# Optimization experiments

Measured on AMD Instinct MI355X. Metric: run time of the kernel, lower is better.

The kernel has to match this reference:

```python
import jax, jax.numpy as jnp
import numpy as np

B, T, H, F = 32, 2048, 1024, 1024  # batch, kv_len, hidden_size, feature_size


def setup_inputs() -> dict:
    key = jax.random.key(0)
    ks = jax.random.split(key, 6)
    s = 0.02  # param init scale
    return {
        "query": jax.random.normal(ks[0], (B, 1, H), jnp.float32),
        "keys": jax.random.normal(ks[1], (B, T, F), jnp.float32),
        "Wa_w": jax.random.normal(ks[2], (H, H), jnp.float32) * s,
        "Wa_b": jnp.zeros((H,), jnp.float32),
        "Ua_w": jax.random.normal(ks[3], (H, F), jnp.float32) * s,
        "Ua_b": jnp.zeros((H,), jnp.float32),
        "Va_w": jax.random.normal(ks[4], (1, H), jnp.float32) * s,
        "Va_b": jnp.zeros((1,), jnp.float32),
    }


def reference(query, keys, Wa_w, Wa_b, Ua_w, Ua_b, Va_w, Va_b):
    # Wa(query): [B,1,H]; Ua(keys): [B,T,H]
    q = jnp.einsum('bqh,oh->bqo', query, Wa_w) + Wa_b
    k = jnp.einsum('btf,of->bto', keys, Ua_w) + Ua_b
    e = jnp.tanh(q + k)                                   # [B,T,H] (broadcast over q dim of size 1)
    scores = jnp.einsum('bth,h->bt', e, Va_w[0]) + Va_b[0]  # Va(...).squeeze(2) -> [B,T]
    scores = scores[:, None, :]                           # unsqueeze(1) -> [B,1,T]
    weights = jax.nn.softmax(scores, axis=-1)             # [B,1,T]
    context = jnp.einsum('bqt,btf->bqf', weights, keys)   # bmm -> [B,1,F]
    return context, weights
```

## Files before the change

### kernel.cpp

```cpp
#include <hip/hip_runtime.h>
#include <hip/hip_bf16.h>

typedef float  f32x4 __attribute__((ext_vector_type(4)));
typedef short  s16x8 __attribute__((ext_vector_type(8)));
typedef __hip_bfloat16 bf16;

#define BDIM 32
#define TDIM 2048
#define HDIM 1024
#define FDIM 1024
#define MTOT (BDIM*TDIM)

#define GLOAD16(gp, lp) __builtin_amdgcn_global_load_lds(                     \
    (const __attribute__((address_space(1))) void*)(gp),                      \
    (__attribute__((address_space(3))) void*)(lp), 16, 0, 0)

#define MFMA_BF16 __builtin_amdgcn_mfma_f32_16x16x32_bf16

__global__ __launch_bounds__(256) void cvt_bf16_kernel(
    const float* __restrict__ src, bf16* __restrict__ dst, int n8)
{
    int i = blockIdx.x * 256 + threadIdx.x;
    const int stride = gridDim.x * 256;
    for (; i < n8; i += stride) {
        const f32x4 a = ((const f32x4*)src)[2 * i];
        const f32x4 b = ((const f32x4*)src)[2 * i + 1];
        union { bf16 h[8]; s16x8 v; } u;
        #pragma unroll
        for (int j = 0; j < 4; ++j) {
            u.h[j]     = __float2bfloat16(a[j]);
            u.h[4 + j] = __float2bfloat16(b[j]);
        }
        ((s16x8*)dst)[i] = u.v;
    }
}

__global__ __launch_bounds__(256) void qeff_kernel(
    const float* __restrict__ query, const float* __restrict__ Wa_w,
    const float* __restrict__ Wa_b,  const float* __restrict__ Ua_b,
    float* __restrict__ qe)
{
    const int lane = threadIdx.x & 63;
    const int gw   = blockIdx.x * 4 + (threadIdx.x >> 6);
    const int b    = gw >> 10;
    const int o    = gw & 1023;
    const float* qp = query + (size_t)b * HDIM;
    const float* wp = Wa_w  + (size_t)o * HDIM;
    float s = 0.f;
    #pragma unroll
    for (int i = 0; i < 16; ++i) {
        const int h = i * 64 + lane;
        s += qp[h] * wp[h];
    }
    #pragma unroll
    for (int off = 32; off > 0; off >>= 1) s += __shfl_down(s, off);
    if (lane == 0) qe[gw] = s + Wa_b[o] + Ua_b[o];
}

#define STAGE_A(buf_, kb_, h_, s_) GLOAD16(                                    \
    Ab + (size_t)(M0 + (h_)*128 + (((s_)>>1)<<4) + srow) * FDIM               \
       + (kb_) + (((s_)&1)<<5) + scg*8,                                        \
    &As[buf_][((((h_)*8 + ((s_)>>1)) * 2 + ((s_)&1)) << 9)])
#define STAGE_B(buf_, kb_, h_, s_) GLOAD16(                                    \
    Bb + (size_t)(N0 + (h_)*128 + (((s_)>>1)<<4) + srow) * FDIM               \
       + (kb_) + (((s_)&1)<<5) + scg*8,                                        \
    &Bs[buf_][((((h_)*8 + ((s_)>>1)) * 2 + ((s_)&1)) << 9)])

__global__ __launch_bounds__(512) void score_gemm_256_kernel(
    const bf16* __restrict__ Ab, const bf16* __restrict__ Bb,
    const float* __restrict__ qe, const float* __restrict__ Va,
    float* __restrict__ scores)
{
    __shared__ bf16 As[2][16384];
    __shared__ bf16 Bs[2][16384];

    const int tid  = threadIdx.x;
    const int lane = tid & 63;
    const int w    = tid >> 6;
    const int wr   = w >> 2;
    const int wc   = w & 3;

    const int bid   = blockIdx.x;
    const int local = bid >> 3;
    const int mt    = (bid & 7) * 32 + (local >> 2);
    const int nt    = local & 3;
    const int M0 = mt * 256, N0 = nt * 256;

    const int srow = lane >> 2;
    const int scg  = (lane & 3) ^ (((lane >> 5) & 1) << 1);
    const int r    = lane & 15;
    const int q4   = lane >> 4;
    const int roff = r * 32 + ((q4 ^ (((r >> 3) & 1) << 1)) & 3) * 8;

    f32x4 acc[8][4];
    #pragma unroll
    for (int m = 0; m < 8; ++m)
        #pragma unroll
        for (int n = 0; n < 4; ++n) acc[m][n] = (f32x4){0.f, 0.f, 0.f, 0.f};

    STAGE_B(0, 0, 0, w); STAGE_B(0, 0, 0, w + 8);
    STAGE_B(0, 0, 1, w); STAGE_B(0, 0, 1, w + 8);
    STAGE_A(0, 0, 0, w); STAGE_A(0, 0, 0, w + 8);
    STAGE_A(0, 0, 1, w); STAGE_A(0, 0, 1, w + 8);
    STAGE_B(1, 64, 0, w); STAGE_B(1, 64, 0, w + 8);
    STAGE_B(1, 64, 1, w); STAGE_B(1, 64, 1, w + 8);
    STAGE_A(1, 64, 0, w); STAGE_A(1, 64, 0, w + 8);
    STAGE_A(1, 64, 1, w); STAGE_A(1, 64, 1, w + 8);
    asm volatile("s_waitcnt vmcnt(8)" ::: "memory");
    __builtin_amdgcn_s_barrier();

    for (int i = 0; i < 8; ++i) {
        const bool pf  = (i < 7);
        const int kbe = (2 * i + 2) << 6;
        const int kbo = (2 * i + 3) << 6;

        s16x8 a0[4][2], a1[4][2], b0[2][2], b1[2][2];

        #pragma unroll
        for (int mf = 0; mf < 4; ++mf)
            #pragma unroll
            for (int ks = 0; ks < 2; ++ks)
                a0[mf][ks] = *(const s16x8*)
                    &As[0][(((wr * 8 + mf) * 2 + ks) << 9) + roff];
        #pragma unroll
        for (int nf = 0; nf < 2; ++nf)
            #pragma unroll
            for (int ks = 0; ks < 2; ++ks)
                b0[nf][ks] = *(const s16x8*)
                    &Bs[0][(((wc * 4 + nf) * 2 + ks) << 9) + roff];
        __builtin_amdgcn_s_barrier();
        __builtin_amdgcn_s_setprio(1);
        #pragma unroll
        for (int mf = 0; mf < 4; ++mf)
            #pragma unroll
            for (int nf = 0; nf < 2; ++nf)
                #pragma unroll
                for (int ks = 0; ks < 2; ++ks)
                    acc[mf][nf] = MFMA_BF16(a0[mf][ks], b0[nf][ks],
                                            acc[mf][nf], 0, 0, 0);
        __builtin_amdgcn_s_setprio(0);
        __builtin_amdgcn_s_barrier();

        #pragma unroll
        for (int nf = 0; nf < 2; ++nf)
            #pragma unroll
            for (int ks = 0; ks < 2; ++ks)
                b1[nf][ks] = *(const s16x8*)
                    &Bs[0][(((wc * 4 + 2 + nf) * 2 + ks) << 9) + roff];
        __builtin_amdgcn_s_barrier();
        __builtin_amdgcn_s_setprio(1);
        #pragma unroll
        for (int mf = 0; mf < 4; ++mf)
            #pragma unroll
            for (int nf = 0; nf < 2; ++nf)
                #pragma unroll
                for (int ks = 0; ks < 2; ++ks)
                    acc[mf][2 + nf] = MFMA_BF16(a0[mf][ks], b1[nf][ks],
                                                acc[mf][2 + nf], 0, 0, 0);
        __builtin_amdgcn_s_setprio(0);
        __builtin_amdgcn_s_barrier();

        #pragma unroll
        for (int mf = 0; mf < 4; ++mf)
            #pragma unroll
            for (int ks = 0; ks < 2; ++ks)
                a1[mf][ks] = *(const s16x8*)
                    &As[0][(((wr * 8 + 4 + mf) * 2 + ks) << 9) + roff];
        if (pf) {
            STAGE_B(0, kbe, 0, w); STAGE_B(0, kbe, 0, w + 8);
            STAGE_B(0, kbe, 1, w); STAGE_B(0, kbe, 1, w + 8);
        }
        __builtin_amdgcn_s_barrier();
        __builtin_amdgcn_s_setprio(1);
        #pragma unroll
        for (int mf = 0; mf < 4; ++mf)
            #pragma unroll
            for (int nf = 0; nf < 2; ++nf)
                #pragma unroll
                for (int ks = 0; ks < 2; ++ks)
                    acc[4 + mf][nf] = MFMA_BF16(a1[mf][ks], b0[nf][ks],
                                                acc[4 + mf][nf], 0, 0, 0);
        __builtin_amdgcn_s_setprio(0);
        __builtin_amdgcn_s_barrier();

        if (pf) {
            STAGE_A(0, kbe, 0, w); STAGE_A(0, kbe, 0, w + 8);
            STAGE_A(0, kbe, 1, w); STAGE_A(0, kbe, 1, w + 8);
        }
        __builtin_amdgcn_s_barrier();
        __builtin_amdgcn_s_setprio(1);
        #pragma unroll
        for (int mf = 0; mf < 4; ++mf)
            #pragma unroll
            for (int nf = 0; nf < 2; ++nf)
                #pragma unroll
                for (int ks = 0; ks < 2; ++ks)
                    acc[4 + mf][2 + nf] = MFMA_BF16(a1[mf][ks], b1[nf][ks],
                                                    acc[4 + mf][2 + nf], 0, 0, 0);
        __builtin_amdgcn_s_setprio(0);
        if (pf) asm volatile("s_waitcnt vmcnt(8)" ::: "memory");
        else    asm volatile("s_waitcnt vmcnt(0)" ::: "memory");
        __builtin_amdgcn_s_barrier();

        #pragma unroll
        for (int mf = 0; mf < 4; ++mf)
            #pragma unroll
            for (int ks = 0; ks < 2; ++ks)
                a0[mf][ks] = *(const s16x8*)
                    &As[1][(((wr * 8 + mf) * 2 + ks) << 9) + roff];
        #pragma unroll
        for (int nf = 0; nf < 2; ++nf)
            #pragma unroll
            for (int ks = 0; ks < 2; ++ks)
                b0[nf][ks] = *(const s16x8*)
                    &Bs[1][(((wc * 4 + nf) * 2 + ks) << 9) + roff];
        __builtin_amdgcn_s_barrier();
        __builtin_amdgcn_s_setprio(1);
        #pragma unroll
        for (int mf = 0; mf < 4; ++mf)
            #pragma unroll
            for (int nf = 0; nf < 2; ++nf)
                #pragma unroll
                for (int ks = 0; ks < 2; ++ks)
                    acc[mf][nf] = MFMA_BF16(a0[mf][ks], b0[nf][ks],
                                            acc[mf][nf], 0, 0, 0);
        __builtin_amdgcn_s_setprio(0);
        __builtin_amdgcn_s_barrier();

        #pragma unroll
        for (int nf = 0; nf < 2; ++nf)
            #pragma unroll
            for (int ks = 0; ks < 2; ++ks)
                b1[nf][ks] = *(const s16x8*)
                    &Bs[1][(((wc * 4 + 2 + nf) * 2 + ks) << 9) + roff];
        __builtin_amdgcn_s_barrier();
        __builtin_amdgcn_s_setprio(1);
        #pragma unroll
        for (int mf = 0; mf < 4; ++mf)
            #pragma unroll
            for (int nf = 0; nf < 2; ++nf)
                #pragma unroll
                for (int ks = 0; ks < 2; ++ks)
                    acc[mf][2 + nf] = MFMA_BF16(a0[mf][ks], b1[nf][ks],
                                                acc[mf][2 + nf], 0, 0, 0);
        __builtin_amdgcn_s_setprio(0);
        __builtin_amdgcn_s_barrier();

        #pragma unroll
        for (int mf = 0; mf < 4; ++mf)
            #pragma unroll
            for (int ks = 0; ks < 2; ++ks)
                a1[mf][ks] = *(const s16x8*)
                    &As[1][(((wr * 8 + 4 + mf) * 2 + ks) << 9) + roff];
        if (pf) {
            STAGE_B(1, kbo, 0, w); STAGE_B(1, kbo, 0, w + 8);
            STAGE_B(1, kbo, 1, w); STAGE_B(1, kbo, 1, w + 8);
        }
        __builtin_amdgcn_s_barrier();
        __builtin_amdgcn_s_setprio(1);
        #pragma unroll
        for (int mf = 0; mf < 4; ++mf)
            #pragma unroll
            for (int nf = 0; nf < 2; ++nf)
                #pragma unroll
                for (int ks = 0; ks < 2; ++ks)
                    acc[4 + mf][nf] = MFMA_BF16(a1[mf][ks], b0[nf][ks],
                                                acc[4 + mf][nf], 0, 0, 0);
        __builtin_amdgcn_s_setprio(0);
        __builtin_amdgcn_s_barrier();

        if (pf) {
            STAGE_A(1, kbo, 0, w); STAGE_A(1, kbo, 0, w + 8);
            STAGE_A(1, kbo, 1, w); STAGE_A(1, kbo, 1, w + 8);
        }
        __builtin_amdgcn_s_barrier();
        __builtin_amdgcn_s_setprio(1);
        #pragma unroll
        for (int mf = 0; mf < 4; ++mf)
            #pragma unroll
            for (int nf = 0; nf < 2; ++nf)
                #pragma unroll
                for (int ks = 0; ks < 2; ++ks)
                    acc[4 + mf][2 + nf] = MFMA_BF16(a1[mf][ks], b1[nf][ks],
                                                    acc[4 + mf][2 + nf], 0, 0, 0);
        __builtin_amdgcn_s_setprio(0);
        if (pf) asm volatile("s_waitcnt vmcnt(8)" ::: "memory");
        __builtin_amdgcn_s_barrier();
    }

    const int b = M0 >> 11;
    const float* qrow = qe + (size_t)b * HDIM;
    #pragma unroll
    for (int mf = 0; mf < 8; ++mf) {
        float part[4] = {0.f, 0.f, 0.f, 0.f};
        #pragma unroll
        for (int nf = 0; nf < 4; ++nf) {
            const int c    = N0 + wc * 64 + nf * 16 + (lane & 15);
            const float va = Va[c];
            const float qv = qrow[c];
            #pragma unroll
            for (int j = 0; j < 4; ++j) {
                const float x = qv + acc[mf][nf][j];
                const float e = __expf(2.0f * x);
                part[j] += va * (1.0f - 2.0f / (e + 1.0f));
            }
        }
        #pragma unroll
        for (int j = 0; j < 4; ++j)
            #pragma unroll
            for (int off = 1; off < 16; off <<= 1)
                part[j] += __shfl_xor(part[j], off);
        if ((lane & 15) == 0) {
            const int rr = M0 + wr * 128 + mf * 16 + (lane >> 4) * 4;
            #pragma unroll
            for (int j = 0; j < 4; ++j) atomicAdd(&scores[rr + j], part[j]);
        }
    }
}

__global__ __launch_bounds__(256) void score_gemm_f32_kernel(
    const float* __restrict__ keys, const float* __restrict__ Ua,
    const float* __restrict__ qe,   const float* __restrict__ Va,
    float* __restrict__ scores)
{
    __shared__ bf16 Asf[128][40];
    __shared__ bf16 Bsf[128][40];

    const int tid  = threadIdx.x;
    const int lane = tid & 63;
    const int wid  = tid >> 6;
    const int wr   = wid >> 1, wc = wid & 1;
    const int n0   = blockIdx.x * 128;
    const int m0   = blockIdx.y * 128;

    const int srow  = tid >> 1;
    const int shalf = tid & 1;
    const float* gA = keys + (size_t)(m0 + srow) * FDIM + shalf * 16;
    const float* gB = Ua   + (size_t)(n0 + srow) * FDIM + shalf * 16;

    f32x4 acc[4][4];
    #pragma unroll
    for (int m = 0; m < 4; ++m)
        #pragma unroll
        for (int n = 0; n < 4; ++n) acc[m][n] = (f32x4){0.f, 0.f, 0.f, 0.f};

    float4 ra[4], rbv[4];
    #pragma unroll
    for (int i = 0; i < 4; ++i) {
        ra[i]  = ((const float4*)gA)[i];
        rbv[i] = ((const float4*)gB)[i];
    }

    for (int kt = 0; kt < 32; ++kt) {
        __syncthreads();
        {
            union { bf16 h[16]; s16x8 v[2]; } ua, ub;
            #pragma unroll
            for (int i = 0; i < 4; ++i) {
                const float* fa = (const float*)&ra[i];
                const float* fb = (const float*)&rbv[i];
                #pragma unroll
                for (int j = 0; j < 4; ++j) {
                    ua.h[i*4+j] = __float2bfloat16(fa[j]);
                    ub.h[i*4+j] = __float2bfloat16(fb[j]);
                }
            }
            *(s16x8*)&Asf[srow][shalf*16]     = ua.v[0];
            *(s16x8*)&Asf[srow][shalf*16 + 8] = ua.v[1];
            *(s16x8*)&Bsf[srow][shalf*16]     = ub.v[0];
            *(s16x8*)&Bsf[srow][shalf*16 + 8] = ub.v[1];
        }
        __syncthreads();

        if (kt + 1 < 32) {
            const float* pa = gA + (kt + 1) * 32;
            const float* pb = gB + (kt + 1) * 32;
            #pragma unroll
            for (int i = 0; i < 4; ++i) {
                ra[i]  = ((const float4*)pa)[i];
                rbv[i] = ((const float4*)pb)[i];
            }
        }

        s16x8 af[4], bfr[4];
        #pragma unroll
        for (int m = 0; m < 4; ++m)
            af[m] = *(const s16x8*)&Asf[wr*64 + m*16 + (lane & 15)][(lane >> 4) * 8];
        #pragma unroll
        for (int n = 0; n < 4; ++n)
            bfr[n] = *(const s16x8*)&Bsf[wc*64 + n*16 + (lane & 15)][(lane >> 4) * 8];
        #pragma unroll
        for (int m = 0; m < 4; ++m)
            #pragma unroll
            for (int n = 0; n < 4; ++n)
                acc[m][n] = MFMA_BF16(af[m], bfr[n], acc[m][n], 0, 0, 0);
    }

    const int b = m0 >> 11;
    const float* qrow = qe + (size_t)b * HDIM;
    #pragma unroll
    for (int m = 0; m < 4; ++m) {
        float part[4] = {0.f, 0.f, 0.f, 0.f};
        #pragma unroll
        for (int n = 0; n < 4; ++n) {
            const int c    = n0 + wc*64 + n*16 + (lane & 15);
            const float va = Va[c];
            const float qv = qrow[c];
            #pragma unroll
            for (int j = 0; j < 4; ++j) {
                const float x = qv + acc[m][n][j];
                const float e = __expf(2.0f * x);
                part[j] += va * (1.0f - 2.0f / (e + 1.0f));
            }
        }
        #pragma unroll
        for (int j = 0; j < 4; ++j)
            #pragma unroll
            for (int off = 1; off < 16; off <<= 1)
                part[j] += __shfl_xor(part[j], off);
        if ((lane & 15) == 0) {
            const int rr = m0 + wr*64 + m*16 + (lane >> 4) * 4;
            #pragma unroll
            for (int j = 0; j < 4; ++j) atomicAdd(&scores[rr + j], part[j]);
        }
    }
}

__global__ __launch_bounds__(256) void softmax_kernel(float* __restrict__ sw)
{
    const int b    = blockIdx.x;
    const int tid  = threadIdx.x;
    const int lane = tid & 63, wid = tid >> 6;
    __shared__ float red[8];

    float v[8];
    float m = -3.4e38f;
    #pragma unroll
    for (int i = 0; i < 8; ++i) {
        v[i] = sw[b * TDIM + i * 256 + tid];
        m = fmaxf(m, v[i]);
    }
    #pragma unroll
    for (int off = 32; off > 0; off >>= 1) m = fmaxf(m, __shfl_xor(m, off));
    if (lane == 0) red[wid] = m;
    __syncthreads();
    m = fmaxf(fmaxf(red[0], red[1]), fmaxf(red[2], red[3]));

    float s = 0.f;
    #pragma unroll
    for (int i = 0; i < 8; ++i) { v[i] = __expf(v[i] - m); s += v[i]; }
    #pragma unroll
    for (int off = 32; off > 0; off >>= 1) s += __shfl_xor(s, off);
    if (lane == 0) red[4 + wid] = s;
    __syncthreads();
    s = (red[4] + red[5]) + (red[6] + red[7]);

    const float inv = 1.0f / s;
    #pragma unroll
    for (int i = 0; i < 8; ++i) sw[b * TDIM + i * 256 + tid] = v[i] * inv;
}

__global__ __launch_bounds__(256) void context_bf16_kernel(
    const bf16* __restrict__ keys, const float* __restrict__ w,
    float* __restrict__ ctx)
{
    const int tc  = blockIdx.x;
    const int b   = blockIdx.y;
    const int tid = threadIdx.x;
    __shared__ float ws_[128];
    if (tid < 128) ws_[tid] = w[b * TDIM + tc * 128 + tid];
    __syncthreads();

    const bf16* kp = keys + ((size_t)b * TDIM + (size_t)tc * 128) * FDIM + tid * 4;
    float4 acc = {0.f, 0.f, 0.f, 0.f};
    #pragma unroll 8
    for (int t = 0; t < 128; ++t) {
        const short4 kv = *(const short4*)(kp + (size_t)t * FDIM);
        const float wt = ws_[t];
        acc.x += wt * __uint_as_float(((unsigned)(unsigned short)kv.x) << 16);
        acc.y += wt * __uint_as_float(((unsigned)(unsigned short)kv.y) << 16);
        acc.z += wt * __uint_as_float(((unsigned)(unsigned short)kv.z) << 16);
        acc.w += wt * __uint_as_float(((unsigned)(unsigned short)kv.w) << 16);
    }
    float* cp = ctx + (size_t)b * FDIM + tid * 4;
    atomicAdd(cp + 0, acc.x); atomicAdd(cp + 1, acc.y);
    atomicAdd(cp + 2, acc.z); atomicAdd(cp + 3, acc.w);
}

__global__ __launch_bounds__(256) void context_f32_kernel(
    const float* __restrict__ keys, const float* __restrict__ w,
    float* __restrict__ ctx)
{
    const int tc  = blockIdx.x;
    const int b   = blockIdx.y;
    const int tid = threadIdx.x;
    __shared__ float ws_[128];
    if (tid < 128) ws_[tid] = w[b * TDIM + tc * 128 + tid];
    __syncthreads();

    const float* kp = keys + ((size_t)b * TDIM + (size_t)tc * 128) * FDIM + tid * 4;
    float4 acc = {0.f, 0.f, 0.f, 0.f};
    #pragma unroll 8
    for (int t = 0; t < 128; ++t) {
        const float4 kv = *(const float4*)(kp + (size_t)t * FDIM);
        const float wt = ws_[t];
        acc.x += wt * kv.x; acc.y += wt * kv.y;
        acc.z += wt * kv.z; acc.w += wt * kv.w;
    }
    float* cp = ctx + (size_t)b * FDIM + tid * 4;
    atomicAdd(cp + 0, acc.x); atomicAdd(cp + 1, acc.y);
    atomicAdd(cp + 2, acc.z); atomicAdd(cp + 3, acc.w);
}

extern "C" void kernel_launch(void* const* d_in, const int* in_sizes, int n_in,
                              void* d_out, int out_size, void* d_ws, size_t ws_size,
                              hipStream_t stream)
{
    const float* query = (const float*)d_in[0];
    const float* keys  = (const float*)d_in[1];
    const float* Wa_w  = (const float*)d_in[2];
    const float* Wa_b  = (const float*)d_in[3];
    const float* Ua_w  = (const float*)d_in[4];
    const float* Ua_b  = (const float*)d_in[5];
    const float* Va_w  = (const float*)d_in[6];

    float* out = (float*)d_out;
    float* ctx = out;
    float* sw  = out + BDIM * HDIM;

    const size_t needA = (size_t)MTOT * FDIM * sizeof(bf16);
    const size_t needB = (size_t)HDIM * FDIM * sizeof(bf16);
    const bool fast = ws_size >= needA + needB;

    hipMemsetAsync(sw, 0, (size_t)BDIM * TDIM * sizeof(float), stream);
    qeff_kernel<<<dim3(BDIM * HDIM / 4), 256, 0, stream>>>(query, Wa_w, Wa_b, Ua_b, ctx);

    if (fast) {
        bf16* Ab = (bf16*)d_ws;
        bf16* Bb = Ab + (size_t)MTOT * FDIM;
        cvt_bf16_kernel<<<dim3(2048), 256, 0, stream>>>(keys, Ab, MTOT * FDIM / 8);
        cvt_bf16_kernel<<<dim3(512),  256, 0, stream>>>(Ua_w, Bb, HDIM * FDIM / 8);
        score_gemm_256_kernel<<<dim3(1024), 512, 0, stream>>>(Ab, Bb, ctx, Va_w, sw);
        softmax_kernel<<<dim3(BDIM), 256, 0, stream>>>(sw);
        hipMemsetAsync(ctx, 0, (size_t)BDIM * HDIM * sizeof(float), stream);
        context_bf16_kernel<<<dim3(16, BDIM), 256, 0, stream>>>(Ab, sw, ctx);
    } else {
        score_gemm_f32_kernel<<<dim3(HDIM / 128, MTOT / 128), 256, 0, stream>>>(
            keys, Ua_w, ctx, Va_w, sw);
        softmax_kernel<<<dim3(BDIM), 256, 0, stream>>>(sw);
        hipMemsetAsync(ctx, 0, (size_t)BDIM * HDIM * sizeof(float), stream);
        context_f32_kernel<<<dim3(16, BDIM), 256, 0, stream>>>(keys, sw, ctx);
    }
}
```

Before: 277.2 us.

## Re-stage GEMM prefetch schedule to spread A and B loads across phases

Reworks the double-buffered LDS prefetch schedule in the fused Ua GEMM. The A tile for the odd stage is now issued during the current iteration's first phases instead of up front, and B and A prefetches for the next stage are split into smaller groups interleaved across the MFMA phases. vmcnt waits are tightened to match, and sched_barriers are added to keep the compiler from reordering across the waits. The aim is to balance global-to-LDS traffic against MFMA work and shorten the prologue, at the cost of more delicate buffer-reuse correctness (As[1] is written while As[0] reads are in flight) and possibly exposed load latency.

```diff
diff --git a/kernel.cpp b/kernel.cpp
--- a/kernel.cpp
+++ b/kernel.cpp
@@ -104,15 +104,14 @@
     STAGE_A(0, 0, 1, w); STAGE_A(0, 0, 1, w + 8);
     STAGE_B(1, 64, 0, w); STAGE_B(1, 64, 0, w + 8);
     STAGE_B(1, 64, 1, w); STAGE_B(1, 64, 1, w + 8);
-    STAGE_A(1, 64, 0, w); STAGE_A(1, 64, 0, w + 8);
-    STAGE_A(1, 64, 1, w); STAGE_A(1, 64, 1, w + 8);
-    asm volatile("s_waitcnt vmcnt(8)" ::: "memory");
+    asm volatile("s_waitcnt vmcnt(4)" ::: "memory");
     __builtin_amdgcn_s_barrier();
 
     for (int i = 0; i < 8; ++i) {
-        const bool pf  = (i < 7);
-        const int kbe = (2 * i + 2) << 6;
-        const int kbo = (2 * i + 3) << 6;
+        const bool pf   = (i < 7);
+        const int kbO1 = (2 * i + 1) << 6;
+        const int kbE2 = (2 * i + 2) << 6;
+        const int kbO2 = (2 * i + 3) << 6;
 
         s16x8 a0[4][2], a1[4][2], b0[2][2], b1[2][2];
 
@@ -128,6 +127,7 @@
             for (int ks = 0; ks < 2; ++ks)
                 b0[nf][ks] = *(const s16x8*)
                     &Bs[0][(((wc * 4 + nf) * 2 + ks) << 9) + roff];
+        STAGE_A(1, kbO1, 0, w); STAGE_A(1, kbO1, 0, w + 8);
         __builtin_amdgcn_s_barrier();
         __builtin_amdgcn_s_setprio(1);
         #pragma unroll
@@ -147,6 +147,7 @@
             for (int ks = 0; ks < 2; ++ks)
                 b1[nf][ks] = *(const s16x8*)
                     &Bs[0][(((wc * 4 + 2 + nf) * 2 + ks) << 9) + roff];
+        STAGE_A(1, kbO1, 1, w); STAGE_A(1, kbO1, 1, w + 8);
         __builtin_amdgcn_s_barrier();
         __builtin_amdgcn_s_setprio(1);
         #pragma unroll
@@ -166,10 +167,7 @@
             for (int ks = 0; ks < 2; ++ks)
                 a1[mf][ks] = *(const s16x8*)
                     &As[0][(((wr * 8 + 4 + mf) * 2 + ks) << 9) + roff];
-        if (pf) {
-            STAGE_B(0, kbe, 0, w); STAGE_B(0, kbe, 0, w + 8);
-            STAGE_B(0, kbe, 1, w); STAGE_B(0, kbe, 1, w + 8);
-        }
+        if (pf) { STAGE_B(0, kbE2, 0, w); STAGE_B(0, kbE2, 0, w + 8); }
         __builtin_amdgcn_s_barrier();
         __builtin_amdgcn_s_setprio(1);
         #pragma unroll
@@ -183,10 +181,7 @@
         __builtin_amdgcn_s_setprio(0);
         __builtin_amdgcn_s_barrier();
 
-        if (pf) {
-            STAGE_A(0, kbe, 0, w); STAGE_A(0, kbe, 0, w + 8);
-            STAGE_A(0, kbe, 1, w); STAGE_A(0, kbe, 1, w + 8);
-        }
+        if (pf) { STAGE_B(0, kbE2, 1, w); STAGE_B(0, kbE2, 1, w + 8); }
         __builtin_amdgcn_s_barrier();
         __builtin_amdgcn_s_setprio(1);
         #pragma unroll
@@ -198,9 +193,10 @@
                     acc[4 + mf][2 + nf] = MFMA_BF16(a1[mf][ks], b1[nf][ks],
                                                     acc[4 + mf][2 + nf], 0, 0, 0);
         __builtin_amdgcn_s_setprio(0);
-        if (pf) asm volatile("s_waitcnt vmcnt(8)" ::: "memory");
+        if (pf) asm volatile("s_waitcnt vmcnt(4)" ::: "memory");
         else    asm volatile("s_waitcnt vmcnt(0)" ::: "memory");
         __builtin_amdgcn_s_barrier();
+        __builtin_amdgcn_sched_barrier(0);
 
         #pragma unroll
         for (int mf = 0; mf < 4; ++mf)
@@ -214,6 +210,7 @@
             for (int ks = 0; ks < 2; ++ks)
                 b0[nf][ks] = *(const s16x8*)
                     &Bs[1][(((wc * 4 + nf) * 2 + ks) << 9) + roff];
+        if (pf) { STAGE_A(0, kbE2, 0, w); STAGE_A(0, kbE2, 0, w + 8); }
         __builtin_amdgcn_s_barrier();
         __builtin_amdgcn_s_setprio(1);
         #pragma unroll
@@ -233,6 +230,7 @@
             for (int ks = 0; ks < 2; ++ks)
                 b1[nf][ks] = *(const s16x8*)
                     &Bs[1][(((wc * 4 + 2 + nf) * 2 + ks) << 9) + roff];
+        if (pf) { STAGE_A(0, kbE2, 1, w); STAGE_A(0, kbE2, 1, w + 8); }
         __builtin_amdgcn_s_barrier();
         __builtin_amdgcn_s_setprio(1);
         #pragma unroll
@@ -252,10 +250,7 @@
             for (int ks = 0; ks < 2; ++ks)
                 a1[mf][ks] = *(const s16x8*)
                     &As[1][(((wr * 8 + 4 + mf) * 2 + ks) << 9) + roff];
-        if (pf) {
-            STAGE_B(1, kbo, 0, w); STAGE_B(1, kbo, 0, w + 8);
-            STAGE_B(1, kbo, 1, w); STAGE_B(1, kbo, 1, w + 8);
-        }
+        if (pf) { STAGE_B(1, kbO2, 0, w); STAGE_B(1, kbO2, 0, w + 8); }
         __builtin_amdgcn_s_barrier();
         __builtin_amdgcn_s_setprio(1);
         #pragma unroll
@@ -269,10 +264,7 @@
         __builtin_amdgcn_s_setprio(0);
         __builtin_amdgcn_s_barrier();
 
-        if (pf) {
-            STAGE_A(1, kbo, 0, w); STAGE_A(1, kbo, 0, w + 8);
-            STAGE_A(1, kbo, 1, w); STAGE_A(1, kbo, 1, w + 8);
-        }
+        if (pf) { STAGE_B(1, kbO2, 1, w); STAGE_B(1, kbO2, 1, w + 8); }
         __builtin_amdgcn_s_barrier();
         __builtin_amdgcn_s_setprio(1);
         #pragma unroll
@@ -284,8 +276,11 @@
                     acc[4 + mf][2 + nf] = MFMA_BF16(a1[mf][ks], b1[nf][ks],
                                                     acc[4 + mf][2 + nf], 0, 0, 0);
         __builtin_amdgcn_s_setprio(0);
-        if (pf) asm volatile("s_waitcnt vmcnt(8)" ::: "memory");
-        __builtin_amdgcn_s_barrier();
+        if (pf) {
+            asm volatile("s_waitcnt vmcnt(4)" ::: "memory");
+            __builtin_amdgcn_s_barrier();
+            __builtin_amdgcn_sched_barrier(0);
+        }
     }
 
     const int b = M0 >> 11;
```

Result: faster. 271.5 us (-2.1%).
